# Kernel tuning notes

Hardware: AMD Instinct MI355X
Metric: run time of the kernel (lower is better)

## Reference

```python
import jax, jax.numpy as jnp
import numpy as np

N, E, IN_DIM, HID, G = 100000, 3200000, 128, 64, 256


def setup_inputs() -> dict:
    key = jax.random.key(0)
    ks = jax.random.split(key, 10)
    x = jax.random.normal(ks[0], (N, IN_DIM), dtype=jnp.float32)
    ei = jax.random.randint(ks[1], (2, E), 0, N, dtype=jnp.int64)
    ew = jax.random.uniform(ks[2], (E,), dtype=jnp.float32)
    batch = jnp.sort(jax.random.randint(ks[3], (N,), 0, G, dtype=jnp.int64))
    W1 = jax.random.normal(ks[4], (IN_DIM, HID), dtype=jnp.float32) * 0.05
    b1 = jnp.zeros((HID,), dtype=jnp.float32)
    W2 = jax.random.normal(ks[5], (HID, HID), dtype=jnp.float32) * 0.05
    b2 = jnp.zeros((HID,), dtype=jnp.float32)
    Wc = jax.random.normal(ks[6], (HID, 1), dtype=jnp.float32) * 0.05
    bc = jnp.zeros((1,), dtype=jnp.float32)
    return {"x": x, "ei": ei, "ew": ew, "batch": batch,
            "W1": W1, "b1": b1, "W2": W2, "b2": b2, "Wc": Wc, "bc": bc}


def _gcn_norm(ei, ew, n):
    # PyG gcn_norm: add self-loops (weight 1), symmetric deg^-1/2 normalization
    loop = jnp.arange(n, dtype=ei.dtype)
    row = jnp.concatenate([ei[0], loop])
    col = jnp.concatenate([ei[1], loop])
    w = jnp.concatenate([ew, jnp.ones((n,), dtype=ew.dtype)])
    deg = jax.ops.segment_sum(w, col, num_segments=n)
    dis = jnp.where(deg > 0, jax.lax.rsqrt(jnp.maximum(deg, 1e-30)), 0.0)
    norm = dis[row] * w * dis[col]
    return row, col, norm


def _gcn_conv(x, row, col, norm, W, b, n):
    xl = x @ W                                   # [N, hid]
    msg = xl[row] * norm[:, None]                # gather + scale, [E+N, hid]
    return jax.ops.segment_sum(msg, col, num_segments=n) + b


def reference(x, ei, ew, batch, W1, b1, W2, b2, Wc, bc):
    n = x.shape[0]
    row, col, norm = _gcn_norm(ei, ew, n)
    h = jax.nn.relu(_gcn_conv(x, row, col, norm, W1, b1, n))
    h = jax.nn.relu(_gcn_conv(h, row, col, norm, W2, b2, n))
    # global mean pool over graphs
    sums = jax.ops.segment_sum(h, batch, num_segments=G)           # [G, hid]
    cnt = jax.ops.segment_sum(jnp.ones((n,), h.dtype), batch, num_segments=G)
    pooled = sums / jnp.maximum(cnt, 1.0)[:, None]
    return (pooled @ Wc + bc).reshape(-1)                           # [G]
```

## Files before the change

### kernel.cpp

```cpp
#include <hip/hip_runtime.h>

#define N_NODES 100000
#define N_PAD   100352
#define N_EDGES 3200000
#define IN_DIM  128
#define HID     64
#define N_GRAPHS 256
#define NB      392
#define NBLK    256
#define EPB     (N_EDGES / NBLK)
#define G1ROWS  32
#define G1BLK   (N_NODES / G1ROWS)

typedef unsigned short ushort_t;
typedef unsigned int   uint_t;

__device__ __forceinline__ ushort_t f2bf(float v) {
    uint_t b = __float_as_uint(v);
    b += 0x7fffu + ((b >> 16) & 1u);
    return (ushort_t)(b >> 16);
}
__device__ __forceinline__ void bf2f2(uint_t u, float& lo, float& hi) {
    lo = __uint_as_float(u << 16);
    hi = __uint_as_float(u & 0xffff0000u);
}
__device__ __forceinline__ void ld_bf16x8(const ushort_t* p, float4& a, float4& b) {
    uint4 u = *(const uint4*)p;
    bf2f2(u.x, a.x, a.y); bf2f2(u.y, a.z, a.w);
    bf2f2(u.z, b.x, b.y); bf2f2(u.w, b.z, b.w);
}
__device__ __forceinline__ void fma8(float4& a0, float4& a1, const uint4& u, float w) {
    float lo, hi;
    bf2f2(u.x, lo, hi); a0.x += lo * w; a0.y += hi * w;
    bf2f2(u.y, lo, hi); a0.z += lo * w; a0.w += hi * w;
    bf2f2(u.z, lo, hi); a1.x += lo * w; a1.y += hi * w;
    bf2f2(u.w, lo, hi); a1.z += lo * w; a1.w += hi * w;
}

__global__ __launch_bounds__(256) void bhist_gemm1_kernel(
        const int* __restrict__ col, int* __restrict__ H,
        const float* __restrict__ x, const float* __restrict__ W1,
        ushort_t* __restrict__ xl) {
    __shared__ float sW[IN_DIM * HID];
    __shared__ float sx[G1ROWS][IN_DIM];
    int tid = threadIdx.x;
    if (blockIdx.x < NBLK) {
        int (*h)[NB] = (int (*)[NB])sW;
        for (int i = tid; i < NB; i += 256) { h[0][i] = 0; h[1][i] = 0; }
        __syncthreads();
        const int4* col4 = (const int4*)col;
        int base4 = blockIdx.x * (EPB / 4);
        int sel = tid & 1;
        for (int j = tid; j < EPB / 4; j += 256) {
            int4 c = col4[base4 + j];
            atomicAdd(&h[sel][c.x >> 8], 1);
            atomicAdd(&h[sel][c.y >> 8], 1);
            atomicAdd(&h[sel][c.z >> 8], 1);
            atomicAdd(&h[sel][c.w >> 8], 1);
        }
        __syncthreads();
        for (int i = tid; i < NB; i += 256) H[i * NBLK + blockIdx.x] = h[0][i] + h[1][i];
    } else {
        int bid = blockIdx.x - NBLK;
        const float4* W4  = (const float4*)W1;
        float4*       sW4 = (float4*)sW;
        #pragma unroll
        for (int i = 0; i < 8; ++i) sW4[tid + 256 * i] = W4[tid + 256 * i];
        int r0 = bid * G1ROWS;
        const float4* x4  = (const float4*)(x + (size_t)r0 * IN_DIM);
        float4*       sx4 = (float4*)&sx[0][0];
        #pragma unroll
        for (int i = 0; i < 4; ++i) sx4[tid + 256 * i] = x4[tid + 256 * i];
        __syncthreads();
        int c  = tid & 63;
        int rb = (tid >> 6) * 8;
        float acc0 = 0.f, acc1 = 0.f, acc2 = 0.f, acc3 = 0.f;
        float acc4 = 0.f, acc5 = 0.f, acc6 = 0.f, acc7 = 0.f;
        #pragma unroll 4
        for (int k4 = 0; k4 < IN_DIM; k4 += 4) {
            float4 x0 = *(const float4*)&sx[rb + 0][k4];
            float4 x1 = *(const float4*)&sx[rb + 1][k4];
            float4 x2 = *(const float4*)&sx[rb + 2][k4];
            float4 x3 = *(const float4*)&sx[rb + 3][k4];
            float4 x4r = *(const float4*)&sx[rb + 4][k4];
            float4 x5 = *(const float4*)&sx[rb + 5][k4];
            float4 x6 = *(const float4*)&sx[rb + 6][k4];
            float4 x7 = *(const float4*)&sx[rb + 7][k4];
            #pragma unroll
            for (int kk = 0; kk < 4; ++kk) {
                float wk = sW[(k4 + kk) * HID + c];
                acc0 += ((const float*)&x0)[kk] * wk;
                acc1 += ((const float*)&x1)[kk] * wk;
                acc2 += ((const float*)&x2)[kk] * wk;
                acc3 += ((const float*)&x3)[kk] * wk;
                acc4 += ((const float*)&x4r)[kk] * wk;
                acc5 += ((const float*)&x5)[kk] * wk;
                acc6 += ((const float*)&x6)[kk] * wk;
                acc7 += ((const float*)&x7)[kk] * wk;
            }
        }
        ushort_t* o = xl + (size_t)(r0 + rb) * HID + c;
        o[0 * HID] = f2bf(acc0);
        o[1 * HID] = f2bf(acc1);
        o[2 * HID] = f2bf(acc2);
        o[3 * HID] = f2bf(acc3);
        o[4 * HID] = f2bf(acc4);
        o[5 * HID] = f2bf(acc5);
        o[6 * HID] = f2bf(acc6);
        o[7 * HID] = f2bf(acc7);
    }
}

__global__ __launch_bounds__(256) void scan1_kernel(int* H, int* __restrict__ bsum) {
    __shared__ int s[256];
    int i = blockIdx.x * 256 + threadIdx.x;
    int v = H[i];
    s[threadIdx.x] = v;
    __syncthreads();
    #pragma unroll
    for (int off = 1; off < 256; off <<= 1) {
        int t = (threadIdx.x >= off) ? s[threadIdx.x - off] : 0;
        __syncthreads();
        s[threadIdx.x] += t;
        __syncthreads();
    }
    H[i] = s[threadIdx.x] - v;
    if (threadIdx.x == 255) bsum[blockIdx.x] = s[255];
}

__global__ __launch_bounds__(256) void bscatter_kernel(const int* __restrict__ row,
                                                       const int* __restrict__ col,
                                                       const float* __restrict__ ew,
                                                       const int* __restrict__ H,
                                                       const int* __restrict__ bsum,
                                                       int* __restrict__ boff,
                                                       int2* __restrict__ recs) {
    __shared__ int2 lrec[EPB];
    __shared__ int  lofs[NB];
    __shared__ int  hcnt[NB];
    __shared__ int  gofs[NB];
    __shared__ int  cur[NB];
    __shared__ int  s[256];
    __shared__ int  carry;
    int tid = threadIdx.x, blk = blockIdx.x;
    if (tid == 0) carry = 0;
    __syncthreads();
    for (int c = 0; c < 2; ++c) {
        int i = c * 256 + tid;
        int v = (i < NB) ? bsum[i] : 0;
        s[tid] = v;
        __syncthreads();
        #pragma unroll
        for (int off = 1; off < 256; off <<= 1) {
            int t = (tid >= off) ? s[tid - off] : 0;
            __syncthreads();
            s[tid] += t;
            __syncthreads();
        }
        if (i < NB) {
            int tb = s[tid] - v + carry;
            int ex = H[i * NBLK + blk];
            gofs[i] = tb + ex;
            hcnt[i] = ((blk < NBLK - 1) ? H[i * NBLK + blk + 1] : v) - ex;
            if (blk == 0) boff[i] = tb;
        }
        __syncthreads();
        if (tid == 0) carry += s[255];
        __syncthreads();
    }
    if (tid == 0) carry = 0;
    __syncthreads();
    for (int c = 0; c < 2; ++c) {
        int i = c * 256 + tid;
        int v = (i < NB) ? hcnt[i] : 0;
        s[tid] = v;
        __syncthreads();
        #pragma unroll
        for (int off = 1; off < 256; off <<= 1) {
            int t = (tid >= off) ? s[tid - off] : 0;
            __syncthreads();
            s[tid] += t;
            __syncthreads();
        }
        if (i < NB) { int l = s[tid] - v + carry; lofs[i] = l; cur[i] = l; }
        __syncthreads();
        if (tid == 0) carry += s[255];
        __syncthreads();
    }
    const int4*   row4 = (const int4*)row;
    const int4*   col4 = (const int4*)col;
    const float4* ew4  = (const float4*)ew;
    int base4 = blk * (EPB / 4);
    for (int j = tid; j < EPB / 4; j += 256) {
        int4   r4 = row4[base4 + j];
        int4   c4 = col4[base4 + j];
        float4 w4 = ew4[base4 + j];
        int p0 = atomicAdd(&cur[c4.x >> 8], 1);
        lrec[p0] = make_int2(r4.x | ((c4.x & 255) << 17), __float_as_int(w4.x));
        int p1 = atomicAdd(&cur[c4.y >> 8], 1);
        lrec[p1] = make_int2(r4.y | ((c4.y & 255) << 17), __float_as_int(w4.y));
        int p2 = atomicAdd(&cur[c4.z >> 8], 1);
        lrec[p2] = make_int2(r4.z | ((c4.z & 255) << 17), __float_as_int(w4.z));
        int p3 = atomicAdd(&cur[c4.w >> 8], 1);
        lrec[p3] = make_int2(r4.w | ((c4.w & 255) << 17), __float_as_int(w4.w));
    }
    __syncthreads();
    int wv = tid >> 6, lane = tid & 63;
    for (int i = wv; i < NB; i += 4) {
        int cnt = hcnt[i], lo = lofs[i], go = gofs[i];
        for (int k = lane; k < cnt; k += 64)
            recs[go + k] = lrec[lo + k];
    }
}

__global__ __launch_bounds__(256) void degcsr_kernel(const int2* __restrict__ recs,
                                                     const int* __restrict__ boff,
                                                     float* __restrict__ dis,
                                                     int* __restrict__ rowptr,
                                                     int2* __restrict__ csr,
                                                     ushort_t* xl) {
    __shared__ int   cnt[256];
    __shared__ float degf[256];
    __shared__ int   sscan[256];
    __shared__ int   cur[256];
    int b = blockIdx.x, tid = threadIdx.x;
    cnt[tid] = 0; degf[tid] = 0.f;
    __syncthreads();
    int s = boff[b], e = (b + 1 < NB) ? boff[b + 1] : N_EDGES;
    for (int j = s + tid; j < e; j += 256) {
        int2 r = recs[j];
        int cl = (r.x >> 17) & 255;
        atomicAdd(&cnt[cl], 1);
        atomicAdd(&degf[cl], __int_as_float(r.y));
    }
    __syncthreads();
    int c = cnt[tid];
    sscan[tid] = c;
    __syncthreads();
    #pragma unroll
    for (int off = 1; off < 256; off <<= 1) {
        int t = (tid >= off) ? sscan[tid - off] : 0;
        __syncthreads();
        sscan[tid] += t;
        __syncthreads();
    }
    int rp = s + sscan[tid] - c;
    rowptr[b * 256 + tid] = rp;
    cur[tid] = rp;
    float d = 1.0f / sqrtf(fmaxf(1.0f + degf[tid], 1e-30f));
    dis[b * 256 + tid] = d;
    __syncthreads();
    degf[tid] = d;
    __syncthreads();
    for (int j = s + tid; j < e; j += 256) {
        int2 r = recs[j];
        int cl = (r.x >> 17) & 255;
        int pos = atomicAdd(&cur[cl], 1);
        csr[pos] = r;
    }
    int n0 = b * 256;
    for (int i = tid; i < 256 * 8; i += 256) {
        int r = i >> 3;
        int n = n0 + r;
        if (n >= N_NODES) break;
        uint4* p = (uint4*)(xl + (size_t)n * HID) + (i & 7);
        float d2 = degf[r];
        uint4 u = *p;
        float lo, hi;
        uint_t w0, w1, w2, w3;
        bf2f2(u.x, lo, hi); w0 = f2bf(lo * d2) | ((uint_t)f2bf(hi * d2) << 16);
        bf2f2(u.y, lo, hi); w1 = f2bf(lo * d2) | ((uint_t)f2bf(hi * d2) << 16);
        bf2f2(u.z, lo, hi); w2 = f2bf(lo * d2) | ((uint_t)f2bf(hi * d2) << 16);
        bf2f2(u.w, lo, hi); w3 = f2bf(lo * d2) | ((uint_t)f2bf(hi * d2) << 16);
        *p = make_uint4(w0, w1, w2, w3);
    }
}

__device__ __forceinline__ void gather_row16(const int2* __restrict__ csr,
                                             const ushort_t* __restrict__ xl,
                                             int base, int end, int n,
                                             int g, int c0,
                                             float4& a0, float4& a1) {
    a0 = make_float4(0.f, 0.f, 0.f, 0.f);
    a1 = make_float4(0.f, 0.f, 0.f, 0.f);
    if (g == 0) {
        ld_bf16x8(xl + (size_t)n * HID + c0, a0, a1);
    }
    int j = base + g;
    for (; j + 14 < end; j += 16) {
        int2 e0 = csr[j];
        int2 e1 = csr[j + 2];
        int2 e2 = csr[j + 4];
        int2 e3 = csr[j + 6];
        int2 e4 = csr[j + 8];
        int2 e5 = csr[j + 10];
        int2 e6 = csr[j + 12];
        int2 e7 = csr[j + 14];
        uint4 u0 = *(const uint4*)(xl + (size_t)(e0.x & 0x1FFFF) * HID + c0);
        uint4 u1 = *(const uint4*)(xl + (size_t)(e1.x & 0x1FFFF) * HID + c0);
        uint4 u2 = *(const uint4*)(xl + (size_t)(e2.x & 0x1FFFF) * HID + c0);
        uint4 u3 = *(const uint4*)(xl + (size_t)(e3.x & 0x1FFFF) * HID + c0);
        uint4 u4 = *(const uint4*)(xl + (size_t)(e4.x & 0x1FFFF) * HID + c0);
        uint4 u5 = *(const uint4*)(xl + (size_t)(e5.x & 0x1FFFF) * HID + c0);
        uint4 u6 = *(const uint4*)(xl + (size_t)(e6.x & 0x1FFFF) * HID + c0);
        uint4 u7 = *(const uint4*)(xl + (size_t)(e7.x & 0x1FFFF) * HID + c0);
        fma8(a0, a1, u0, __int_as_float(e0.y));
        fma8(a0, a1, u1, __int_as_float(e1.y));
        fma8(a0, a1, u2, __int_as_float(e2.y));
        fma8(a0, a1, u3, __int_as_float(e3.y));
        fma8(a0, a1, u4, __int_as_float(e4.y));
        fma8(a0, a1, u5, __int_as_float(e5.y));
        fma8(a0, a1, u6, __int_as_float(e6.y));
        fma8(a0, a1, u7, __int_as_float(e7.y));
    }
    for (; j + 6 < end; j += 8) {
        int2 e0 = csr[j];
        int2 e1 = csr[j + 2];
        int2 e2 = csr[j + 4];
        int2 e3 = csr[j + 6];
        uint4 u0 = *(const uint4*)(xl + (size_t)(e0.x & 0x1FFFF) * HID + c0);
        uint4 u1 = *(const uint4*)(xl + (size_t)(e1.x & 0x1FFFF) * HID + c0);
        uint4 u2 = *(const uint4*)(xl + (size_t)(e2.x & 0x1FFFF) * HID + c0);
        uint4 u3 = *(const uint4*)(xl + (size_t)(e3.x & 0x1FFFF) * HID + c0);
        fma8(a0, a1, u0, __int_as_float(e0.y));
        fma8(a0, a1, u1, __int_as_float(e1.y));
        fma8(a0, a1, u2, __int_as_float(e2.y));
        fma8(a0, a1, u3, __int_as_float(e3.y));
    }
    for (; j < end; j += 2) {
        int2 e0 = csr[j];
        uint4 u0 = *(const uint4*)(xl + (size_t)(e0.x & 0x1FFFF) * HID + c0);
        fma8(a0, a1, u0, __int_as_float(e0.y));
    }
    a0.x += __shfl_down(a0.x, 8, 64); a0.y += __shfl_down(a0.y, 8, 64);
    a0.z += __shfl_down(a0.z, 8, 64); a0.w += __shfl_down(a0.w, 8, 64);
    a1.x += __shfl_down(a1.x, 8, 64); a1.y += __shfl_down(a1.y, 8, 64);
    a1.z += __shfl_down(a1.z, 8, 64); a1.w += __shfl_down(a1.w, 8, 64);
}

__global__ __launch_bounds__(256) void gather_gemm2_kernel(
        const int2* __restrict__ csr, const int* __restrict__ rowptr,
        const float* __restrict__ dis, const ushort_t* __restrict__ xl,
        const float* __restrict__ W2, const float* __restrict__ b1,
        ushort_t* __restrict__ xl2) {
    __shared__ float sW[HID * HID];
    __shared__ float sh[16][HID + 4];
    int tid = threadIdx.x;
    const float4* W4  = (const float4*)W2;
    float4*       sW4 = (float4*)sW;
    #pragma unroll
    for (int i = 0; i < 4; ++i) sW4[tid + 256 * i] = W4[tid + 256 * i];

    int n0   = blockIdx.x * 16;
    int wv   = tid >> 6;
    int lane = tid & 63;
    int lr   = wv * 4 + (lane >> 4);
    int n    = n0 + lr;
    int g    = (lane >> 3) & 1;
    int c0   = (lane & 7) << 3;
    int base = rowptr[n], end = rowptr[n + 1];
    float d  = dis[n];
    float4 a0, a1;
    gather_row16(csr, xl, base, end, n, g, c0, a0, a1);
    if (g == 0) {
        float4 bb0 = *(const float4*)(b1 + c0);
        float4 bb1 = *(const float4*)(b1 + c0 + 4);
        float4 h0 = make_float4(fmaxf(a0.x * d + bb0.x, 0.f), fmaxf(a0.y * d + bb0.y, 0.f),
                                fmaxf(a0.z * d + bb0.z, 0.f), fmaxf(a0.w * d + bb0.w, 0.f));
        float4 h1 = make_float4(fmaxf(a1.x * d + bb1.x, 0.f), fmaxf(a1.y * d + bb1.y, 0.f),
                                fmaxf(a1.z * d + bb1.z, 0.f), fmaxf(a1.w * d + bb1.w, 0.f));
        *(float4*)(&sh[lr][c0])     = h0;
        *(float4*)(&sh[lr][c0 + 4]) = h1;
    }
    __syncthreads();
    int cc = tid & 63, rq = tid >> 6;
    float acc0 = 0.f, acc1 = 0.f, acc2 = 0.f, acc3 = 0.f;
    #pragma unroll 8
    for (int k = 0; k < HID; ++k) {
        float wk = sW[k * HID + cc];
        acc0 += sh[rq * 4 + 0][k] * wk;
        acc1 += sh[rq * 4 + 1][k] * wk;
        acc2 += sh[rq * 4 + 2][k] * wk;
        acc3 += sh[rq * 4 + 3][k] * wk;
    }
    xl2[(size_t)(n0 + rq * 4 + 0) * HID + cc] = f2bf(acc0 * dis[n0 + rq * 4 + 0]);
    xl2[(size_t)(n0 + rq * 4 + 1) * HID + cc] = f2bf(acc1 * dis[n0 + rq * 4 + 1]);
    xl2[(size_t)(n0 + rq * 4 + 2) * HID + cc] = f2bf(acc2 * dis[n0 + rq * 4 + 2]);
    xl2[(size_t)(n0 + rq * 4 + 3) * HID + cc] = f2bf(acc3 * dis[n0 + rq * 4 + 3]);
}

__global__ __launch_bounds__(256) void gather_pool_kernel(
        const int2* __restrict__ csr, const int* __restrict__ rowptr,
        const float* __restrict__ dis, const ushort_t* __restrict__ xl,
        const float* __restrict__ b2, const float* __restrict__ Wc,
        float* __restrict__ sval) {
    int tid  = threadIdx.x;
    int n    = (blockIdx.x * 256 + tid) >> 4;
    int lane = tid & 63;
    int g    = (lane >> 3) & 1;
    int c0   = (lane & 7) << 3;
    int base = rowptr[n], end = rowptr[n + 1];
    float d  = dis[n];
    float4 a0, a1;
    gather_row16(csr, xl, base, end, n, g, c0, a0, a1);
    float4 bb0 = *(const float4*)(b2 + c0);
    float4 bb1 = *(const float4*)(b2 + c0 + 4);
    float4 wc0 = *(const float4*)(Wc + c0);
    float4 wc1 = *(const float4*)(Wc + c0 + 4);
    float s = fmaxf(a0.x * d + bb0.x, 0.f) * wc0.x + fmaxf(a0.y * d + bb0.y, 0.f) * wc0.y
            + fmaxf(a0.z * d + bb0.z, 0.f) * wc0.z + fmaxf(a0.w * d + bb0.w, 0.f) * wc0.w
            + fmaxf(a1.x * d + bb1.x, 0.f) * wc1.x + fmaxf(a1.y * d + bb1.y, 0.f) * wc1.y
            + fmaxf(a1.z * d + bb1.z, 0.f) * wc1.z + fmaxf(a1.w * d + bb1.w, 0.f) * wc1.w;
    s += __shfl_down(s, 4, 64);
    s += __shfl_down(s, 2, 64);
    s += __shfl_down(s, 1, 64);
    if ((lane & 15) == 0) sval[n] = s;
}

__global__ __launch_bounds__(256) void final_out_kernel(const float* __restrict__ sval,
                                                        const int* __restrict__ batch,
                                                        const float* __restrict__ bc,
                                                        float* __restrict__ out) {
    __shared__ float s[256];
    int g = blockIdx.x;
    int lo = 0, hi = N_NODES;
    while (lo < hi) { int m = (lo + hi) >> 1; if (batch[m] < g) lo = m + 1; else hi = m; }
    int start = lo;
    hi = N_NODES;
    while (lo < hi) { int m = (lo + hi) >> 1; if (batch[m] < g + 1) lo = m + 1; else hi = m; }
    int end = lo;
    float acc = 0.f;
    for (int i = start + threadIdx.x; i < end; i += 256) acc += sval[i];
    s[threadIdx.x] = acc;
    __syncthreads();
    #pragma unroll
    for (int off = 128; off > 0; off >>= 1) {
        if (threadIdx.x < off) s[threadIdx.x] += s[threadIdx.x + off];
        __syncthreads();
    }
    if (threadIdx.x == 0)
        out[g] = s[0] / fmaxf((float)(end - start), 1.0f) + bc[0];
}

extern "C" void kernel_launch(void* const* d_in, const int* in_sizes, int n_in,
                              void* d_out, int out_size, void* d_ws, size_t ws_size,
                              hipStream_t stream) {
    const float* x     = (const float*)d_in[0];
    const int*   ei    = (const int*)  d_in[1];
    const float* ew    = (const float*)d_in[2];
    const int*   batch = (const int*)  d_in[3];
    const float* W1    = (const float*)d_in[4];
    const float* b1    = (const float*)d_in[5];
    const float* W2    = (const float*)d_in[6];
    const float* b2    = (const float*)d_in[7];
    const float* Wc    = (const float*)d_in[8];
    const float* bc    = (const float*)d_in[9];
    float* out = (float*)d_out;

    const int* row = ei;
    const int* col = ei + N_EDGES;

    int2*     recs   = (int2*)d_ws;
    ushort_t* xlA    = (ushort_t*)(recs + N_EDGES);
    ushort_t* xlB    = xlA + (size_t)N_NODES * HID;
    int2*     csr    = (int2*)(xlB + (size_t)N_NODES * HID);
    int*      rowptr = (int*)(csr + N_EDGES);
    float*    dis    = (float*)(rowptr + N_PAD);
    int*      bsum   = (int*)(dis + N_PAD);
    int*      boff   = bsum + 512;
    float*    sval   = (float*)(boff + 512);
    int*      H      = (int*)csr;

    bhist_gemm1_kernel<<<NBLK + G1BLK, 256, 0, stream>>>(col, H, x, W1, xlA);
    scan1_kernel    <<<NB,   256, 0, stream>>>(H, bsum);
    bscatter_kernel <<<NBLK, 256, 0, stream>>>(row, col, ew, H, bsum, boff, recs);
    degcsr_kernel   <<<NB,   256, 0, stream>>>(recs, boff, dis, rowptr, csr, xlA);
    gather_gemm2_kernel<<<N_NODES / 16, 256, 0, stream>>>(csr, rowptr, dis, xlA, W2, b1, xlB);
    gather_pool_kernel <<<N_NODES / 16, 256, 0, stream>>>(csr, rowptr, dis, xlB, b2, Wc, sval);
    final_out_kernel<<<N_GRAPHS, 256, 0, stream>>>(sval, batch, bc, out);
}
```

Baseline: 369.0 us.

## Cooperatively load CSR records and software-pipeline gather in double-buffered blocks

The row gather now splits each node's edge range into two contiguous halves, one per 8-lane group. Within a group, 4 lanes load CSR records in parallel and broadcast them with shuffles, replacing the per-lane strided record loads. The loop is software-pipelined: the next block's records and feature rows are fetched while the current block is accumulated, using 32-bit address arithmetic. This aims to cut redundant CSR loads and expose more memory-level parallelism. The cost is extra shuffles, clamped padding loads for short rows, and higher register pressure.

```diff
diff --git a/kernel.cpp b/kernel.cpp
--- a/kernel.cpp
+++ b/kernel.cpp
@@ -35,6 +35,11 @@
     bf2f2(u.y, lo, hi); a0.z += lo * w; a0.w += hi * w;
     bf2f2(u.z, lo, hi); a1.x += lo * w; a1.y += hi * w;
     bf2f2(u.w, lo, hi); a1.z += lo * w; a1.w += hi * w;
+}
+__device__ __forceinline__ int2 ldrec(const int2* __restrict__ csr, int last, int idx) {
+    int2 r = csr[idx <= last ? idx : last];
+    if (idx > last) r.y = 0;
+    return r;
 }
 
 __global__ __launch_bounds__(256) void bhist_gemm1_kernel(
@@ -279,58 +284,59 @@
 __device__ __forceinline__ void gather_row16(const int2* __restrict__ csr,
                                              const ushort_t* __restrict__ xl,
                                              int base, int end, int n,
-                                             int g, int c0,
+                                             int g, int c0, int lane,
                                              float4& a0, float4& a1) {
     a0 = make_float4(0.f, 0.f, 0.f, 0.f);
     a1 = make_float4(0.f, 0.f, 0.f, 0.f);
     if (g == 0) {
-        ld_bf16x8(xl + (size_t)n * HID + c0, a0, a1);
-    }
-    int j = base + g;
-    for (; j + 14 < end; j += 16) {
-        int2 e0 = csr[j];
-        int2 e1 = csr[j + 2];
-        int2 e2 = csr[j + 4];
-        int2 e3 = csr[j + 6];
-        int2 e4 = csr[j + 8];
-        int2 e5 = csr[j + 10];
-        int2 e6 = csr[j + 12];
-        int2 e7 = csr[j + 14];
-        uint4 u0 = *(const uint4*)(xl + (size_t)(e0.x & 0x1FFFF) * HID + c0);
-        uint4 u1 = *(const uint4*)(xl + (size_t)(e1.x & 0x1FFFF) * HID + c0);
-        uint4 u2 = *(const uint4*)(xl + (size_t)(e2.x & 0x1FFFF) * HID + c0);
-        uint4 u3 = *(const uint4*)(xl + (size_t)(e3.x & 0x1FFFF) * HID + c0);
-        uint4 u4 = *(const uint4*)(xl + (size_t)(e4.x & 0x1FFFF) * HID + c0);
-        uint4 u5 = *(const uint4*)(xl + (size_t)(e5.x & 0x1FFFF) * HID + c0);
-        uint4 u6 = *(const uint4*)(xl + (size_t)(e6.x & 0x1FFFF) * HID + c0);
-        uint4 u7 = *(const uint4*)(xl + (size_t)(e7.x & 0x1FFFF) * HID + c0);
-        fma8(a0, a1, u0, __int_as_float(e0.y));
-        fma8(a0, a1, u1, __int_as_float(e1.y));
-        fma8(a0, a1, u2, __int_as_float(e2.y));
-        fma8(a0, a1, u3, __int_as_float(e3.y));
-        fma8(a0, a1, u4, __int_as_float(e4.y));
-        fma8(a0, a1, u5, __int_as_float(e5.y));
-        fma8(a0, a1, u6, __int_as_float(e6.y));
-        fma8(a0, a1, u7, __int_as_float(e7.y));
-    }
-    for (; j + 6 < end; j += 8) {
-        int2 e0 = csr[j];
-        int2 e1 = csr[j + 2];
-        int2 e2 = csr[j + 4];
-        int2 e3 = csr[j + 6];
-        uint4 u0 = *(const uint4*)(xl + (size_t)(e0.x & 0x1FFFF) * HID + c0);
-        uint4 u1 = *(const uint4*)(xl + (size_t)(e1.x & 0x1FFFF) * HID + c0);
-        uint4 u2 = *(const uint4*)(xl + (size_t)(e2.x & 0x1FFFF) * HID + c0);
-        uint4 u3 = *(const uint4*)(xl + (size_t)(e3.x & 0x1FFFF) * HID + c0);
-        fma8(a0, a1, u0, __int_as_float(e0.y));
-        fma8(a0, a1, u1, __int_as_float(e1.y));
-        fma8(a0, a1, u2, __int_as_float(e2.y));
-        fma8(a0, a1, u3, __int_as_float(e3.y));
-    }
-    for (; j < end; j += 2) {
-        int2 e0 = csr[j];
-        uint4 u0 = *(const uint4*)(xl + (size_t)(e0.x & 0x1FFFF) * HID + c0);
-        fma8(a0, a1, u0, __int_as_float(e0.y));
+        ld_bf16x8(xl + (uint_t)(n * HID + c0), a0, a1);
+    }
+    int tot  = end - base;
+    int half = (tot + 1) >> 1;
+    int gs   = base + (g ? half : 0);
+    int m    = g ? (tot - half) : half;
+    if (m > 0) {
+        int last = gs + m - 1;
+        int li4  = lane & 3;
+        int gb   = lane & 56;
+        int nb   = (m + 3) >> 2;
+
+#define BCI(r_, u0_, u1_, u2_, u3_, w0_, w1_, w2_, w3_) do {                     \
+        int r0_ = __shfl((r_).x, gb + 0, 64), r1_ = __shfl((r_).x, gb + 1, 64);  \
+        int r2_ = __shfl((r_).x, gb + 2, 64), r3_ = __shfl((r_).x, gb + 3, 64);  \
+        w0_ = __int_as_float(__shfl((r_).y, gb + 0, 64));                         \
+        w1_ = __int_as_float(__shfl((r_).y, gb + 1, 64));                         \
+        w2_ = __int_as_float(__shfl((r_).y, gb + 2, 64));                         \
+        w3_ = __int_as_float(__shfl((r_).y, gb + 3, 64));                         \
+        u0_ = *(const uint4*)(xl + (uint_t)((r0_ & 0x1FFFF) * HID + c0));         \
+        u1_ = *(const uint4*)(xl + (uint_t)((r1_ & 0x1FFFF) * HID + c0));         \
+        u2_ = *(const uint4*)(xl + (uint_t)((r2_ & 0x1FFFF) * HID + c0));         \
+        u3_ = *(const uint4*)(xl + (uint_t)((r3_ & 0x1FFFF) * HID + c0));         \
+    } while (0)
+
+        uint4 uA0, uA1, uA2, uA3, uB0, uB1, uB2, uB3;
+        float wA0, wA1, wA2, wA3, wB0, wB1, wB2, wB3;
+        int2 rA = ldrec(csr, last, gs + li4);
+        int2 rB = (nb > 1) ? ldrec(csr, last, gs + 4 + li4) : rA;
+        BCI(rA, uA0, uA1, uA2, uA3, wA0, wA1, wA2, wA3);
+        int blk = 0;
+        while (true) {
+            bool hasB  = (blk + 1 < nb);
+            bool hasA2 = (blk + 2 < nb);
+            if (hasA2) rA = ldrec(csr, last, gs + (blk + 2) * 4 + li4);
+            if (hasB) { BCI(rB, uB0, uB1, uB2, uB3, wB0, wB1, wB2, wB3); }
+            fma8(a0, a1, uA0, wA0); fma8(a0, a1, uA1, wA1);
+            fma8(a0, a1, uA2, wA2); fma8(a0, a1, uA3, wA3);
+            if (!hasB) break;
+            bool hasB2 = (blk + 3 < nb);
+            if (hasB2) rB = ldrec(csr, last, gs + (blk + 3) * 4 + li4);
+            if (hasA2) { BCI(rA, uA0, uA1, uA2, uA3, wA0, wA1, wA2, wA3); }
+            fma8(a0, a1, uB0, wB0); fma8(a0, a1, uB1, wB1);
+            fma8(a0, a1, uB2, wB2); fma8(a0, a1, uB3, wB3);
+            if (!hasA2) break;
+            blk += 2;
+        }
+#undef BCI
     }
     a0.x += __shfl_down(a0.x, 8, 64); a0.y += __shfl_down(a0.y, 8, 64);
     a0.z += __shfl_down(a0.z, 8, 64); a0.w += __shfl_down(a0.w, 8, 64);
@@ -361,7 +367,7 @@
     int base = rowptr[n], end = rowptr[n + 1];
     float d  = dis[n];
     float4 a0, a1;
-    gather_row16(csr, xl, base, end, n, g, c0, a0, a1);
+    gather_row16(csr, xl, base, end, n, g, c0, lane, a0, a1);
     if (g == 0) {
         float4 bb0 = *(const float4*)(b1 + c0);
         float4 bb1 = *(const float4*)(b1 + c0 + 4);
@@ -402,7 +408,7 @@
     int base = rowptr[n], end = rowptr[n + 1];
     float d  = dis[n];
     float4 a0, a1;
-    gather_row16(csr, xl, base, end, n, g, c0, a0, a1);
+    gather_row16(csr, xl, base, end, n, g, c0, lane, a0, a1);
     float4 bb0 = *(const float4*)(b2 + c0);
     float4 bb1 = *(const float4*)(b2 + c0 + 4);
     float4 wc0 = *(const float4*)(Wc + c0);
```

Result: faster. 360.5 us (-2.3%).
